# Performance work log

Measured on AMD Instinct MI355X. Metric: run time of the kernel, lower is better.

The kernel has to match this reference:

```python
import jax, jax.numpy as jnp
import numpy as np

B, T, C = 4, 4096, 1024


def setup_inputs() -> dict:
    key = jax.random.key(0)
    k1, k2, k3 = jax.random.split(key, 3)
    x = jax.random.normal(k1, (B, T, C), dtype=jnp.float32)
    # causal mask (attn positions where mask==0 are set to -inf, as in masked_fill)
    mask = jnp.tril(jnp.ones((T, T), dtype=bool))
    # torch nn.Linear weights: y = x @ W.T ; scale like default init
    w_qkv = jax.random.normal(k2, (3 * C, C), dtype=jnp.float32) * (C ** -0.5)
    w_out = jax.random.normal(k3, (C, C), dtype=jnp.float32) * (C ** -0.5)
    return {"x": x, "mask": mask, "w_qkv": w_qkv, "w_out": w_out}


def reference(x, mask, w_qkv, w_out):
    scale = C ** -0.5
    qkv = jnp.einsum("btc,dc->btd", x, w_qkv)          # [B,T,3C]
    q, k, v = jnp.split(qkv, 3, axis=-1)                 # each [B,T,C]
    attn = jnp.einsum("btc,bsc->bts", q, k) * scale      # [B,T,T]
    attn = jnp.where(mask, attn, -jnp.inf)               # masked_fill(mask==0, -inf)
    attn = jax.nn.softmax(attn, axis=-1)
    out = jnp.einsum("bts,bsc->btc", attn, v)            # [B,T,C]
    return jnp.einsum("btc,dc->btd", out, w_out)
```

## Files before the change

### kernel.cpp

```cpp
#include <hip/hip_runtime.h>


typedef unsigned short u16;
typedef float f32x4 __attribute__((ext_vector_type(4)));
typedef __bf16 bf16x8 __attribute__((ext_vector_type(8)));

__device__ __forceinline__ u16 f2bf(float f) {
  __bf16 h = (__bf16)f;
  return __builtin_bit_cast(u16, h);
}

__device__ __forceinline__ void lds_barrier() {
  asm volatile("s_waitcnt lgkmcnt(0)" ::: "memory");
  __builtin_amdgcn_s_barrier();
}

__global__ __launch_bounds__(256) void cvt_bf16(const float* __restrict__ src,
                                                u16* __restrict__ dst, int n8) {
  const int i = blockIdx.x * 256 + threadIdx.x;
  if (i < n8) {
    float4 a = ((const float4*)src)[2 * i];
    float4 b = ((const float4*)src)[2 * i + 1];
    u16 t[8] = {f2bf(a.x), f2bf(a.y), f2bf(a.z), f2bf(a.w),
                f2bf(b.x), f2bf(b.y), f2bf(b.z), f2bf(b.w)};
    ((uint4*)dst)[i] = *(const uint4*)t;
  }
}

template <typename TA, typename TB, typename TC, int MODE>
__global__ __launch_bounds__(256) void gemm_bt(const TA* __restrict__ A,
                                               const TB* __restrict__ B,
                                               TC* __restrict__ C,
                                               int M, int N, int K) {
  constexpr int LDT = 40;
  __shared__ u16 As[128 * LDT];
  __shared__ u16 Bs[128 * LDT];
  __shared__ __align__(16) char Craw[34816];
  const int tid = threadIdx.x;
  const int lane = tid & 63, wv = tid >> 6;
  const int l15 = lane & 15, l4 = lane >> 4;
  const int bm = blockIdx.y * 128, bn = blockIdx.x * 128;
  const int wm = (wv >> 1) * 64, wn = (wv & 1) * 64;
  const int srow = tid >> 1, scol = (tid & 1) * 16;
  const TA* ag = A + (size_t)(bm + srow) * K + scol;
  const TB* bg = B + (size_t)(bn + srow) * K + scol;

  uint4 pau[2], pbu[2];
  auto loadA = [&](int off) {
    pau[0] = *(const uint4*)((const u16*)ag + off);
    pau[1] = *(const uint4*)((const u16*)ag + off + 8);
  };
  auto loadB = [&](int off) {
    pbu[0] = *(const uint4*)((const u16*)bg + off);
    pbu[1] = *(const uint4*)((const u16*)bg + off + 8);
  };

  f32x4 acc[4][4] = {};
  loadA(0);
  loadB(0);

  for (int k0 = 0; k0 < K; k0 += 32) {
    __syncthreads();
    *(uint4*)&As[srow * LDT + scol] = pau[0];
    *(uint4*)&As[srow * LDT + scol + 8] = pau[1];
    *(uint4*)&Bs[srow * LDT + scol] = pbu[0];
    *(uint4*)&Bs[srow * LDT + scol + 8] = pbu[1];
    __syncthreads();
    if (k0 + 32 < K) {
      loadA(k0 + 32);
      loadB(k0 + 32);
    }
    bf16x8 af[4], bfr[4];
#pragma unroll
    for (int t = 0; t < 4; ++t)
      af[t] = *(const bf16x8*)&As[(wm + t * 16 + l15) * LDT + l4 * 8];
#pragma unroll
    for (int t = 0; t < 4; ++t)
      bfr[t] = *(const bf16x8*)&Bs[(wn + t * 16 + l15) * LDT + l4 * 8];
#pragma unroll
    for (int mt = 0; mt < 4; ++mt)
#pragma unroll
      for (int nt = 0; nt < 4; ++nt)
        acc[mt][nt] = __builtin_amdgcn_mfma_f32_16x16x32_bf16(af[mt], bfr[nt], acc[mt][nt], 0, 0, 0);
  }

  if constexpr (MODE == 1) {
    u16(*Cs)[136] = (u16(*)[136])Craw;
    __syncthreads();
#pragma unroll
    for (int mt = 0; mt < 4; ++mt)
#pragma unroll
      for (int nt = 0; nt < 4; ++nt)
#pragma unroll
        for (int r = 0; r < 4; ++r)
          Cs[wm + mt * 16 + l4 * 4 + r][wn + nt * 16 + l15] = f2bf(acc[mt][nt][r]);
    __syncthreads();
    const int region = bn >> 10;
    if (region != 1) {
      u16* dst = (region == 0) ? (u16*)C : ((u16*)C + 33554432);
      const int cb = bn & 1023;
#pragma unroll
      for (int i = 0; i < 8; ++i) {
        const int row = i * 16 + (tid >> 4);
        const int c8 = (tid & 15) * 8;
        uint4 v = *(const uint4*)&Cs[row][c8];
        *(uint4*)(dst + (size_t)(bm + row) * 1024 + cb + c8) = v;
      }
    } else {
      u16* K4 = (u16*)C + 16777216;
      const int b_ = blockIdx.y >> 5;
      const int s16b = (blockIdx.y & 31) * 8;
      const int d32b = ((bn - 1024) >> 5);
      const int l63 = tid & 63;
#pragma unroll
      for (int p = 0; p < 8; ++p) {
        const int fid = p * 4 + (tid >> 6);
        const int s16l = fid >> 2, d32l = fid & 3;
        uint4 v = *(const uint4*)&Cs[s16l * 16 + (l63 & 15)][d32l * 32 + (l63 >> 4) * 8];
        *(uint4*)(K4 + ((size_t)((b_ * 256 + s16b + s16l) * 32 + d32b + d32l)) * 512 + l63 * 8) = v;
      }
    }
  } else {
    float(*Csf)[132] = (float(*)[132])Craw;
#pragma unroll 1
    for (int h = 0; h < 2; ++h) {
      __syncthreads();
      if ((wv >> 1) == h) {
#pragma unroll
        for (int mt = 0; mt < 4; ++mt)
#pragma unroll
          for (int nt = 0; nt < 4; ++nt)
#pragma unroll
            for (int r = 0; r < 4; ++r)
              Csf[mt * 16 + l4 * 4 + r][wn + nt * 16 + l15] = acc[mt][nt][r];
      }
      __syncthreads();
#pragma unroll
      for (int i = 0; i < 8; ++i) {
        const int k = i * 256 + tid;
        const int row = k >> 5, cg = (k & 31) * 4;
        float4 v = *(const float4*)&Csf[row][cg];
        *(float4*)((float*)C + (size_t)(bm + h * 64 + row) * N + bn + cg) = v;
      }
    }
  }
}

__global__ __launch_bounds__(256) void transpose_v4(const u16* __restrict__ Vb,
                                                    u16* __restrict__ V4) {
  __shared__ u16 Ts[64][72];
  const int b = blockIdx.z;
  const int s0 = blockIdx.x * 64, c0 = blockIdx.y * 64;
  const int tid = threadIdx.x;
#pragma unroll
  for (int i = 0; i < 2; ++i) {
    const int k = tid + 256 * i;
    const int sr = k >> 3, c8 = (k & 7) * 8;
    uint4 val = *(const uint4*)(Vb + ((size_t)(b * 4096 + s0 + sr)) * 1024 + c0 + c8);
    const u16* e = (const u16*)&val;
#pragma unroll
    for (int j = 0; j < 8; ++j) Ts[c8 + j][sr] = e[j];
  }
  __syncthreads();
#pragma unroll
  for (int i = 0; i < 2; ++i) {
    const int k = tid + 256 * i;
    const int cr = k >> 3, s8 = (k & 7) * 8;
    uint4 val = *(const uint4*)&Ts[cr][s8];
    const int c = c0 + cr, s = s0 + s8;
    const int lane = (((s >> 3) & 3) << 4) + (c & 15);
    const size_t idx = ((size_t)((b * 64 + (c >> 4)) * 128 + (s >> 5))) * 512 + lane * 8;
    *(uint4*)(V4 + idx) = val;
  }
}

__global__ __launch_bounds__(512, 2) void flash_attn(const u16* __restrict__ Qb,
                                                     const u16* __restrict__ K4,
                                                     const u16* __restrict__ V4,
                                                     u16* __restrict__ ao) {
  __shared__ float Sred[8][32][40];
  __shared__ u16 P[32][40];
  __shared__ float Al[32];

  const int tid = threadIdx.x;
  const int lane = tid & 63;
  const int ds = tid >> 6;
  const int l15 = lane & 15, l4 = lane >> 4;
  const int lane8 = lane * 8;
  const int b = blockIdx.x & 3;
  const int ii = (blockIdx.x >> 2) & 63;
  const int half = blockIdx.x >> 8;
  const size_t base = (size_t)b * 4096;
  const int srow = ds * 4 + l4;
  const int rswz = (ds & 3) << 3;
  const int wswz = l4 << 3;

  const int qt = half ? (127 - ii) : ii;
  const int t0 = qt * 32;

  bf16x8 qf[2][4];
#pragma unroll
  for (int rg = 0; rg < 2; ++rg)
#pragma unroll
    for (int kb = 0; kb < 4; ++kb)
      qf[rg][kb] = *(const bf16x8*)(Qb + (base + t0 + rg * 16 + l15) * 1024 +
                                    ds * 128 + kb * 32 + l4 * 8);

  f32x4 acc[2][8] = {};
  float m_run = -1e30f;
  float l_run = 0.0f;

  bf16x8 kcur[8], knxt[8];
  {
    const int s0p = half ? t0 : 0;
    const size_t kb0 = ((size_t)((b * 256 + (s0p >> 4)) * 32 + ds * 4)) * 512 + lane8;
#pragma unroll
    for (int nt = 0; nt < 2; ++nt)
#pragma unroll
      for (int kb = 0; kb < 4; ++kb)
        kcur[nt * 4 + kb] = *(const bf16x8*)(K4 + kb0 + nt * 16384 + kb * 512);
  }

  const int n_tiles = qt + 1;
  for (int j = 0; j < n_tiles; ++j) {
    const int it = half ? (qt - j) : j;
    const int s0 = it * 32;
    const int itn = half ? (it > 0 ? it - 1 : 0) : (it < qt ? it + 1 : qt);
    const int s0n = itn * 32;

    bf16x8 vf[8];
    {
      const size_t vb0 = ((size_t)((b * 64 + ds * 8) * 128 + (s0 >> 5))) * 512 + lane8;
#pragma unroll
      for (int nt = 0; nt < 8; ++nt)
        vf[nt] = *(const bf16x8*)(V4 + vb0 + nt * 65536);
    }
    {
      const size_t kbn = ((size_t)((b * 256 + (s0n >> 4)) * 32 + ds * 4)) * 512 + lane8;
#pragma unroll
      for (int nt = 0; nt < 2; ++nt)
#pragma unroll
        for (int kb = 0; kb < 4; ++kb)
          knxt[nt * 4 + kb] = *(const bf16x8*)(K4 + kbn + nt * 16384 + kb * 512);
    }

    f32x4 sp[2][2] = {};
#pragma unroll
    for (int kb = 0; kb < 4; ++kb)
#pragma unroll
      for (int nt = 0; nt < 2; ++nt)
#pragma unroll
        for (int rg = 0; rg < 2; ++rg)
          sp[rg][nt] = __builtin_amdgcn_mfma_f32_16x16x32_bf16(qf[rg][kb], kcur[nt * 4 + kb],
                                                               sp[rg][nt], 0, 0, 0);
#pragma unroll
    for (int rg = 0; rg < 2; ++rg)
#pragma unroll
      for (int nt = 0; nt < 2; ++nt)
#pragma unroll
        for (int r = 0; r < 4; ++r)
          Sred[ds][rg * 16 + l4 * 4 + r][(nt * 16 + l15) ^ wswz] = sp[rg][nt][r];
    lds_barrier();

    {
      float sa = 0.0f, sb = 0.0f;
#pragma unroll
      for (int w2 = 0; w2 < 8; ++w2) {
        sa += Sred[w2][srow][l15 ^ rswz];
        sb += Sred[w2][srow][(l15 + 16) ^ rswz];
      }
      sa *= 0.03125f;
      sb *= 0.03125f;
      if (s0 + l15 > t0 + srow) sa = -1e30f;
      if (s0 + l15 + 16 > t0 + srow) sb = -1e30f;
      float mt_ = fmaxf(sa, sb);
      mt_ = fmaxf(mt_, __shfl_xor(mt_, 1));
      mt_ = fmaxf(mt_, __shfl_xor(mt_, 2));
      mt_ = fmaxf(mt_, __shfl_xor(mt_, 4));
      mt_ = fmaxf(mt_, __shfl_xor(mt_, 8));
      const float mn = fmaxf(m_run, mt_);
      const float al = __expf(m_run - mn);
      m_run = mn;
      const float pa = __expf(sa - mn);
      const float pb = __expf(sb - mn);
      float ls = pa + pb;
      ls += __shfl_xor(ls, 1);
      ls += __shfl_xor(ls, 2);
      ls += __shfl_xor(ls, 4);
      ls += __shfl_xor(ls, 8);
      l_run = al * l_run + ls;
      P[srow][l15] = f2bf(pa);
      P[srow][l15 + 16] = f2bf(pb);
      Al[srow] = al;
    }
    lds_barrier();

    float av[2][4];
    int need = 0;
#pragma unroll
    for (int rg = 0; rg < 2; ++rg)
#pragma unroll
      for (int r = 0; r < 4; ++r) {
        av[rg][r] = Al[rg * 16 + l4 * 4 + r];
        need |= (av[rg][r] != 1.0f) ? 1 : 0;
      }
    if (__any(need)) {
#pragma unroll
      for (int rg = 0; rg < 2; ++rg)
#pragma unroll
        for (int nt = 0; nt < 8; ++nt)
#pragma unroll
          for (int r = 0; r < 4; ++r) acc[rg][nt][r] *= av[rg][r];
    }

    bf16x8 pf[2];
#pragma unroll
    for (int rg = 0; rg < 2; ++rg)
      pf[rg] = *(const bf16x8*)&P[rg * 16 + l15][l4 * 8];
#pragma unroll
    for (int nt = 0; nt < 8; ++nt)
#pragma unroll
      for (int rg = 0; rg < 2; ++rg)
        acc[rg][nt] = __builtin_amdgcn_mfma_f32_16x16x32_bf16(pf[rg], vf[nt], acc[rg][nt], 0, 0, 0);

#pragma unroll
    for (int q8 = 0; q8 < 8; ++q8) kcur[q8] = knxt[q8];
  }

  __syncthreads();
  if (l15 == 0) Al[srow] = 1.0f / l_run;
  __syncthreads();
  float iv[2][4];
#pragma unroll
  for (int rg = 0; rg < 2; ++rg)
#pragma unroll
    for (int r = 0; r < 4; ++r) iv[rg][r] = Al[rg * 16 + l4 * 4 + r];
#pragma unroll
  for (int rg = 0; rg < 2; ++rg)
#pragma unroll
    for (int nt = 0; nt < 8; ++nt) {
      const size_t rbase = (base + t0 + rg * 16 + l4 * 4) * 1024 + ds * 128 + nt * 16 + l15;
#pragma unroll
      for (int r = 0; r < 4; ++r)
        ao[rbase + (size_t)r * 1024] = f2bf(acc[rg][nt][r] * iv[rg][r]);
    }
}

extern "C" void kernel_launch(void* const* d_in, const int* in_sizes, int n_in,
                              void* d_out, int out_size, void* d_ws, size_t ws_size,
                              hipStream_t stream) {
  const float* x     = (const float*)d_in[0];
  const float* w_qkv = (const float*)d_in[2];
  const float* w_out = (const float*)d_in[3];
  float* out = (float*)d_out;

  u16* ws  = (u16*)d_ws;
  u16* Qb  = ws;
  u16* K4p = ws + 16777216;
  u16* Vb  = ws + 33554432;
  u16* V4p = ws + 50331648;
  u16* aop = ws + 67108864;
  u16* xb  = aop;
  u16* wqb = V4p;
  u16* wob = Vb;

  cvt_bf16<<<dim3(8192), 256, 0, stream>>>(x, xb, 2097152);
  cvt_bf16<<<dim3(1536), 256, 0, stream>>>(w_qkv, wqb, 393216);
  gemm_bt<u16, u16, u16, 1><<<dim3(24, 128), 256, 0, stream>>>(xb, wqb, Qb, 16384, 3072, 1024);
  transpose_v4<<<dim3(64, 16, 4), 256, 0, stream>>>(Vb, V4p);
  cvt_bf16<<<dim3(512), 256, 0, stream>>>(w_out, wob, 131072);
  flash_attn<<<dim3(512), 512, 0, stream>>>(Qb, K4p, V4p, aop);
  gemm_bt<u16, u16, float, 0><<<dim3(8, 128), 256, 0, stream>>>(aop, wob, out, 16384, 1024, 1024);
}
```

Before: 735.3 us.

## Stage GEMM tiles with direct global-to-LDS loads and double buffering

The bf16 GEMM kernel no longer stages tiles through registers before writing them to LDS. It now issues global_load_lds 16-byte loads straight into a double-buffered, unpadded LDS tile. This leaves one barrier per k-step and lets the load of the next tile overlap the MFMA work on the current one. The cost is that the 40-element row padding is gone, so LDS fragment reads may hit more bank conflicts. Correctness also now depends on the barrier waiting for the async LDS loads to complete.

```diff
diff --git a/kernel.cpp b/kernel.cpp
--- a/kernel.cpp
+++ b/kernel.cpp
@@ -13,6 +13,11 @@
 __device__ __forceinline__ void lds_barrier() {
   asm volatile("s_waitcnt lgkmcnt(0)" ::: "memory");
   __builtin_amdgcn_s_barrier();
+}
+
+__device__ __forceinline__ void glds16(const u16* g, u16* l) {
+  __builtin_amdgcn_global_load_lds((const __attribute__((address_space(1))) void*)g,
+                                   (__attribute__((address_space(3))) void*)l, 16, 0, 0);
 }
 
 __global__ __launch_bounds__(256) void cvt_bf16(const float* __restrict__ src,
@@ -27,65 +32,62 @@
   }
 }
 
-template <typename TA, typename TB, typename TC, int MODE>
-__global__ __launch_bounds__(256) void gemm_bt(const TA* __restrict__ A,
-                                               const TB* __restrict__ B,
+template <typename TC, int MODE>
+__global__ __launch_bounds__(256) void gemm_bt(const u16* __restrict__ A,
+                                               const u16* __restrict__ B,
                                                TC* __restrict__ C,
                                                int M, int N, int K) {
-  constexpr int LDT = 40;
-  __shared__ u16 As[128 * LDT];
-  __shared__ u16 Bs[128 * LDT];
-  __shared__ __align__(16) char Craw[34816];
+  __shared__ __align__(16) char pool[36864];
+  u16* Asb = (u16*)pool;
+  u16* Bsb = (u16*)(pool + 16384);
+
   const int tid = threadIdx.x;
   const int lane = tid & 63, wv = tid >> 6;
   const int l15 = lane & 15, l4 = lane >> 4;
   const int bm = blockIdx.y * 128, bn = blockIdx.x * 128;
   const int wm = (wv >> 1) * 64, wn = (wv & 1) * 64;
-  const int srow = tid >> 1, scol = (tid & 1) * 16;
-  const TA* ag = A + (size_t)(bm + srow) * K + scol;
-  const TB* bg = B + (size_t)(bn + srow) * K + scol;
-
-  uint4 pau[2], pbu[2];
-  auto loadA = [&](int off) {
-    pau[0] = *(const uint4*)((const u16*)ag + off);
-    pau[1] = *(const uint4*)((const u16*)ag + off + 8);
+
+  const int c0 = 2 * wv, c1 = 2 * wv + 1;
+  const int gr0 = 16 * c0 + (lane >> 2), gr1 = 16 * c1 + (lane >> 2);
+  const int gcol = (lane & 3) * 8;
+  const u16* a0 = A + (size_t)(bm + gr0) * K + gcol;
+  const u16* a1 = A + (size_t)(bm + gr1) * K + gcol;
+  const u16* b0 = B + (size_t)(bn + gr0) * K + gcol;
+  const u16* b1 = B + (size_t)(bn + gr1) * K + gcol;
+
+  auto stage = [&](int buf, int k0) {
+    glds16(a0 + k0, Asb + buf * 4096 + c0 * 512);
+    glds16(a1 + k0, Asb + buf * 4096 + c1 * 512);
+    glds16(b0 + k0, Bsb + buf * 4096 + c0 * 512);
+    glds16(b1 + k0, Bsb + buf * 4096 + c1 * 512);
   };
-  auto loadB = [&](int off) {
-    pbu[0] = *(const uint4*)((const u16*)bg + off);
-    pbu[1] = *(const uint4*)((const u16*)bg + off + 8);
-  };
 
   f32x4 acc[4][4] = {};
-  loadA(0);
-  loadB(0);
+  int cur = 0;
+  stage(0, 0);
 
   for (int k0 = 0; k0 < K; k0 += 32) {
     __syncthreads();
-    *(uint4*)&As[srow * LDT + scol] = pau[0];
-    *(uint4*)&As[srow * LDT + scol + 8] = pau[1];
-    *(uint4*)&Bs[srow * LDT + scol] = pbu[0];
-    *(uint4*)&Bs[srow * LDT + scol + 8] = pbu[1];
-    __syncthreads();
-    if (k0 + 32 < K) {
-      loadA(k0 + 32);
-      loadB(k0 + 32);
-    }
+    if (k0 + 32 < K) stage(cur ^ 1, k0 + 32);
+    const u16* Ab = Asb + cur * 4096;
+    const u16* Bb = Bsb + cur * 4096;
     bf16x8 af[4], bfr[4];
 #pragma unroll
     for (int t = 0; t < 4; ++t)
-      af[t] = *(const bf16x8*)&As[(wm + t * 16 + l15) * LDT + l4 * 8];
+      af[t] = *(const bf16x8*)&Ab[(wm + t * 16 + l15) * 32 + l4 * 8];
 #pragma unroll
     for (int t = 0; t < 4; ++t)
-      bfr[t] = *(const bf16x8*)&Bs[(wn + t * 16 + l15) * LDT + l4 * 8];
+      bfr[t] = *(const bf16x8*)&Bb[(wn + t * 16 + l15) * 32 + l4 * 8];
 #pragma unroll
     for (int mt = 0; mt < 4; ++mt)
 #pragma unroll
       for (int nt = 0; nt < 4; ++nt)
         acc[mt][nt] = __builtin_amdgcn_mfma_f32_16x16x32_bf16(af[mt], bfr[nt], acc[mt][nt], 0, 0, 0);
+    cur ^= 1;
   }
 
   if constexpr (MODE == 1) {
-    u16(*Cs)[136] = (u16(*)[136])Craw;
+    u16(*Cs)[136] = (u16(*)[136])pool;
     __syncthreads();
 #pragma unroll
     for (int mt = 0; mt < 4; ++mt)
@@ -121,7 +123,7 @@
       }
     }
   } else {
-    float(*Csf)[132] = (float(*)[132])Craw;
+    float(*Csf)[132] = (float(*)[132])pool;
 #pragma unroll 1
     for (int h = 0; h < 2; ++h) {
       __syncthreads();
@@ -366,9 +368,9 @@
 
   cvt_bf16<<<dim3(8192), 256, 0, stream>>>(x, xb, 2097152);
   cvt_bf16<<<dim3(1536), 256, 0, stream>>>(w_qkv, wqb, 393216);
-  gemm_bt<u16, u16, u16, 1><<<dim3(24, 128), 256, 0, stream>>>(xb, wqb, Qb, 16384, 3072, 1024);
+  gemm_bt<u16, 1><<<dim3(24, 128), 256, 0, stream>>>(xb, wqb, Qb, 16384, 3072, 1024);
   transpose_v4<<<dim3(64, 16, 4), 256, 0, stream>>>(Vb, V4p);
   cvt_bf16<<<dim3(512), 256, 0, stream>>>(w_out, wob, 131072);
   flash_attn<<<dim3(512), 512, 0, stream>>>(Qb, K4p, V4p, aop);
-  gemm_bt<u16, u16, float, 0><<<dim3(8, 128), 256, 0, stream>>>(aop, wob, out, 16384, 1024, 1024);
-}
+  gemm_bt<float, 0><<<dim3(8, 128), 256, 0, stream>>>(aop, wob, out, 16384, 1024, 1024);
+}
```

After: 589.8 us. 19.8% less time.
